# Kernel optimization log

Measured on AMD Instinct MI355X. Metric: run time of the kernel, lower is better.

## Reference

```python
import jax, jax.numpy as jnp
import numpy as np

HEADS = 8
DIM_HEAD = 64
SCALE = DIM_HEAD ** -0.5


def setup_inputs() -> dict:
    key = jax.random.key(0)
    ks = jax.random.split(key, 6)
    b, dim, h, w = 8, 512, 64, 64
    ctx_dim, n = 768, 256
    inner = HEADS * DIM_HEAD  # 512
    x = jax.random.normal(ks[0], (b, dim, h, w), jnp.float32)
    context = jax.random.normal(ks[1], (b, n, ctx_dim), jnp.float32)
    # 1x1 convs / linear reduced to [out, in] matrices
    Wq = jax.random.normal(ks[2], (inner, dim), jnp.float32) * 0.02
    Wkv = jax.random.normal(ks[3], (2 * inner, ctx_dim), jnp.float32) * 0.02
    Wout = jax.random.normal(ks[4], (dim, inner), jnp.float32) * 0.02
    bout = jnp.zeros((dim,), jnp.float32)
    return {"x": x, "context": context, "Wq": Wq, "Wkv": Wkv, "Wout": Wout, "bout": bout}


def reference(x, context, Wq, Wkv, Wout, bout):
    b, c, h, w = x.shape
    # to_q: 1x1 conv (no bias) == per-pixel channel matmul
    q = jnp.einsum('bcxy,ec->bexy', x, Wq)              # [b, inner, h, w]
    # rearrange 'b (h d) x y -> b h (x y) d'
    q = q.reshape(b, HEADS, DIM_HEAD, h * w).transpose(0, 1, 3, 2)
    # to_kv: Linear(context_dim -> 2*inner, no bias)
    kv = jnp.einsum('bnc,ec->bne', context, Wkv)        # [b, n, 2*inner]
    k, v = jnp.split(kv, 2, axis=-1)
    # rearrange 'b n (h d) -> b h n d'
    n = context.shape[1]
    k = k.reshape(b, n, HEADS, DIM_HEAD).transpose(0, 2, 1, 3)
    v = v.reshape(b, n, HEADS, DIM_HEAD).transpose(0, 2, 1, 3)
    sim = jnp.einsum('bhid,bhjd->bhij', q, k) * SCALE   # [b, h, hw, n]
    attn = jax.nn.softmax(sim, axis=-1)
    out = jnp.einsum('bhij,bhjd->bhid', attn, v)        # [b, h, hw, d]
    # rearrange 'b h (x y) d -> b (h d) x y'
    out = out.transpose(0, 1, 3, 2).reshape(b, HEADS * DIM_HEAD, h, w)
    # to_out: 1x1 conv with bias, plus residual
    out = jnp.einsum('bexy,ce->bcxy', out, Wout) + bout[None, :, None, None]
    return out + x
```

## Files before the change

### kernel.cpp

```cpp
#include <hip/hip_runtime.h>

typedef unsigned short u16;
typedef __bf16 bf16x8 __attribute__((ext_vector_type(8)));
typedef __bf16 bf16x4 __attribute__((ext_vector_type(4)));
typedef float f32x4 __attribute__((ext_vector_type(4)));

__device__ __forceinline__ u16 f2bf(float f) {
  __bf16 h = (__bf16)f;
  return *(u16*)&h;
}

__device__ __forceinline__ f32x4 mfma16(bf16x8 a, bf16x8 b, f32x4 c) {
  return __builtin_amdgcn_mfma_f32_16x16x32_bf16(a, b, c, 0, 0, 0);
}

__device__ __forceinline__ void async16(void* lds, const void* g) {
  __builtin_amdgcn_global_load_lds(
      (const __attribute__((address_space(1))) unsigned int*)g,
      (__attribute__((address_space(3))) unsigned int*)lds, 16, 0, 0);
}

#define QSCALE 0.18033688011112042f

__global__ __launch_bounds__(256) void prep_cast(
    const float* __restrict__ Wq, const float* __restrict__ Wkv,
    const float* __restrict__ Wout, const float* __restrict__ ctx,
    u16* __restrict__ Wq_b, u16* __restrict__ Wkv_b,
    u16* __restrict__ Wout_b, u16* __restrict__ ctx_b) {
  const long NWQ = 512L * 512, NWKV = 1024L * 768, NWOUT = 512L * 512, NCTX = 2048L * 768;
  const long total = NWQ + NWKV + NWOUT + NCTX;
  long stride = (long)gridDim.x * 256;
  for (long i = (long)blockIdx.x * 256 + threadIdx.x; i < total; i += stride) {
    long j = i;
    if (j < NWQ) { Wq_b[j] = f2bf(Wq[j] * QSCALE); continue; }
    j -= NWQ;
    if (j < NWKV) { Wkv_b[j] = f2bf(Wkv[j]); continue; }
    j -= NWKV;
    if (j < NWOUT) { Wout_b[j] = f2bf(Wout[j]); continue; }
    j -= NWOUT;
    ctx_b[j] = f2bf(ctx[j]);
  }
}

__global__ __launch_bounds__(256) void transpose_x(const float* __restrict__ x,
                                                   u16* __restrict__ xT) {
  __shared__ float tile[64][65];
  const int b = blockIdx.z, p0 = blockIdx.x * 64, c0 = blockIdx.y * 64;
  const int tx = threadIdx.x & 63, ty = threadIdx.x >> 6;
  const float* xb = x + (long)b * (512L * 4096);
  #pragma unroll
  for (int i = ty; i < 64; i += 4)
    tile[i][tx] = xb[(long)(c0 + i) * 4096 + p0 + tx];
  __syncthreads();
  u16* xTb = xT + (long)b * (4096L * 512);
  #pragma unroll
  for (int i = ty; i < 64; i += 4)
    xTb[(long)(p0 + i) * 512 + c0 + tx] = f2bf(tile[tx][i]);
}

__global__ __launch_bounds__(256) void transpose_v(const u16* __restrict__ kv,
                                                   u16* __restrict__ vT) {
  __shared__ u16 tile[64][65];
  const int b = blockIdx.z, e0 = blockIdx.x * 64, n0 = blockIdx.y * 64;
  const int tx = threadIdx.x & 63, ty = threadIdx.x >> 6;
  #pragma unroll
  for (int i = ty; i < 64; i += 4)
    tile[i][tx] = kv[(long)(b * 256 + n0 + i) * 1024 + 512 + e0 + tx];
  __syncthreads();
  #pragma unroll
  for (int i = ty; i < 64; i += 4)
    vT[(long)b * (512L * 256) + (long)(e0 + i) * 256 + n0 + tx] = tile[tx][i];
}

__global__ __launch_bounds__(256) void gemm_nt128(
    const u16* __restrict__ A, const u16* __restrict__ B, u16* __restrict__ C,
    int M, int N, int K) {
  __shared__ u16 ldsA[2][128 * 64];
  __shared__ u16 ldsB[2][128 * 64];
  const int t = threadIdx.x, wv = t >> 6, ln = t & 63;
  const int m0 = blockIdx.x * 128, n0 = blockIdx.y * 128;
  const int wr = wv >> 1, wc = wv & 1, fr = ln & 15, fq = ln >> 4;

  const u16* aSrc[4];
  const u16* bSrc[4];
  int lbase[4];
  #pragma unroll
  for (int i = 0; i < 4; i++) {
    int c = i * 256 + wv * 64 + ln;
    int row = c >> 3, slot = (c & 7) ^ (row & 7);
    aSrc[i] = A + (long)(m0 + row) * K + slot * 8;
    bSrc[i] = B + (long)(n0 + row) * K + slot * 8;
    lbase[i] = (i * 256 + wv * 64) * 8;
  }

  f32x4 acc[4][4] = {};
  const int nk = K >> 6;
  int cur = 0;

  #pragma unroll
  for (int i = 0; i < 4; i++) {
    async16(&ldsA[0][lbase[i]], aSrc[i]);
    async16(&ldsB[0][lbase[i]], bSrc[i]);
  }

  for (int kt = 0; kt < nk; ++kt) {
    __syncthreads();
    if (kt + 1 < nk) {
      const int ko = (kt + 1) * 64;
      #pragma unroll
      for (int i = 0; i < 4; i++) {
        async16(&ldsA[cur ^ 1][lbase[i]], aSrc[i] + ko);
        async16(&ldsB[cur ^ 1][lbase[i]], bSrc[i] + ko);
      }
    }
    const char* Ab = (const char*)ldsA[cur];
    const char* Bb = (const char*)ldsB[cur];
    #pragma unroll
    for (int kk = 0; kk < 2; ++kk) {
      bf16x8 a[4], b[4];
      #pragma unroll
      for (int mf = 0; mf < 4; ++mf) {
        int row = wr * 64 + mf * 16 + fr;
        a[mf] = *(const bf16x8*)(Ab + row * 128 +
                                 ((kk * 64 + fq * 16) ^ ((row & 7) << 4)));
      }
      #pragma unroll
      for (int nf = 0; nf < 4; ++nf) {
        int row = wc * 64 + nf * 16 + fr;
        b[nf] = *(const bf16x8*)(Bb + row * 128 +
                                 ((kk * 64 + fq * 16) ^ ((row & 7) << 4)));
      }
      #pragma unroll
      for (int mf = 0; mf < 4; ++mf)
        #pragma unroll
        for (int nf = 0; nf < 4; ++nf)
          acc[mf][nf] = mfma16(a[mf], b[nf], acc[mf][nf]);
    }
    cur ^= 1;
  }

  #pragma unroll
  for (int mf = 0; mf < 4; ++mf)
    #pragma unroll
    for (int r = 0; r < 4; ++r) {
      int grow = m0 + wr * 64 + mf * 16 + fq * 4 + r;
      #pragma unroll
      for (int nf = 0; nf < 4; ++nf) {
        int gcol = n0 + wc * 64 + nf * 16 + fr;
        C[(long)grow * N + gcol] = f2bf(acc[mf][nf][r]);
      }
    }
}

template <int EPI>
__global__ __launch_bounds__(512, 2) void gemm_nt256(
    const u16* __restrict__ A, const u16* __restrict__ B, void* __restrict__ Cv,
    int M, int N, int K, long aStrideZ, long bStrideZ, long cStrideZ,
    const float* __restrict__ bias, const float* __restrict__ resid) {
  __shared__ u16 ldsA[2][256 * 64];
  __shared__ u16 ldsB[2][256 * 64];
  const int t = threadIdx.x, wv = t >> 6, ln = t & 63;
  const int m0 = blockIdx.x * 256, n0 = blockIdx.y * 256, z = blockIdx.z;
  const u16* Az = A + (long)z * aStrideZ;
  const u16* Bz = B + (long)z * bStrideZ;
  const int wr = wv >> 2, wc = wv & 3, fr = ln & 15, fq = ln >> 4;

  const u16* aSrc[4];
  const u16* bSrc[4];
  int lbase[4];
  #pragma unroll
  for (int i = 0; i < 4; i++) {
    int c = i * 512 + wv * 64 + ln;
    int row = c >> 3, slot = (c & 7) ^ (row & 7);
    aSrc[i] = Az + (long)(m0 + row) * K + slot * 8;
    bSrc[i] = Bz + (long)(n0 + row) * K + slot * 8;
    lbase[i] = (i * 512 + wv * 64) * 8;
  }

  f32x4 acc[8][4] = {};
  const int nk = K >> 6;
  int cur = 0;

  #pragma unroll
  for (int i = 0; i < 4; i++) {
    async16(&ldsA[0][lbase[i]], aSrc[i]);
    async16(&ldsB[0][lbase[i]], bSrc[i]);
  }

  for (int kt = 0; kt < nk; ++kt) {
    if (kt + 1 < nk) {
      const int ko = (kt + 1) * 64;
      #pragma unroll
      for (int i = 0; i < 4; i++) {
        async16(&ldsA[cur ^ 1][lbase[i]], aSrc[i] + ko);
        async16(&ldsB[cur ^ 1][lbase[i]], bSrc[i] + ko);
      }
      asm volatile("s_waitcnt vmcnt(8)" ::: "memory");
    } else {
      asm volatile("s_waitcnt vmcnt(0)" ::: "memory");
    }
    __builtin_amdgcn_s_barrier();
    __builtin_amdgcn_sched_barrier(0);

    const char* Ab = (const char*)ldsA[cur];
    const char* Bb = (const char*)ldsB[cur];
    #pragma unroll
    for (int kk = 0; kk < 2; ++kk) {
      bf16x8 a[8], b[4];
      #pragma unroll
      for (int mf = 0; mf < 8; ++mf) {
        int row = wr * 128 + mf * 16 + fr;
        a[mf] = *(const bf16x8*)(Ab + row * 128 +
                                 ((kk * 64 + fq * 16) ^ ((row & 7) << 4)));
      }
      #pragma unroll
      for (int nf = 0; nf < 4; ++nf) {
        int row = wc * 64 + nf * 16 + fr;
        b[nf] = *(const bf16x8*)(Bb + row * 128 +
                                 ((kk * 64 + fq * 16) ^ ((row & 7) << 4)));
      }
      __builtin_amdgcn_s_setprio(1);
      #pragma unroll
      for (int mf = 0; mf < 8; ++mf)
        #pragma unroll
        for (int nf = 0; nf < 4; ++nf)
          acc[mf][nf] = mfma16(a[mf], b[nf], acc[mf][nf]);
      __builtin_amdgcn_s_setprio(0);
    }

    __builtin_amdgcn_sched_barrier(0);
    __builtin_amdgcn_s_barrier();
    cur ^= 1;
  }

  if (EPI == 0) {
    u16* Cb = (u16*)Cv + (long)z * cStrideZ;
    #pragma unroll
    for (int mf = 0; mf < 8; ++mf)
      #pragma unroll
      for (int r = 0; r < 4; ++r) {
        int grow = m0 + wr * 128 + mf * 16 + fq * 4 + r;
        #pragma unroll
        for (int nf = 0; nf < 4; ++nf) {
          int gcol = n0 + wc * 64 + nf * 16 + fr;
          Cb[(long)grow * N + gcol] = f2bf(acc[mf][nf][r]);
        }
      }
  } else {
    float* Cf = (float*)Cv + (long)z * cStrideZ;
    const float* Rz = resid + (long)z * cStrideZ;
    #pragma unroll
    for (int mf = 0; mf < 8; ++mf)
      #pragma unroll
      for (int r = 0; r < 4; ++r) {
        int grow = m0 + wr * 128 + mf * 16 + fq * 4 + r;
        float bv = bias[grow];
        #pragma unroll
        for (int nf = 0; nf < 4; ++nf) {
          int gcol = n0 + wc * 64 + nf * 16 + fr;
          long idx = (long)grow * N + gcol;
          Cf[idx] = acc[mf][nf][r] + bv + Rz[idx];
        }
      }
  }
}

__global__ __launch_bounds__(512) void attn_kernel(
    const u16* __restrict__ q, const u16* __restrict__ kv,
    const u16* __restrict__ vT, u16* __restrict__ ao) {
  __shared__ u16 klds[256 * 64];
  __shared__ u16 vlds[64 * 256];
  __shared__ u16 plds[128 * 256];
  const int t = threadIdx.x, w = t >> 6, ln = t & 63;
  const int fr = ln & 15, fq = ln >> 4;
  const int p0 = blockIdx.x * 1024, h = blockIdx.y, b = blockIdx.z;

  const u16* kb = kv + (long)b * 256 * 1024 + h * 64;
  const u16* vb = vT + (long)b * (512L * 256) + (long)h * 64 * 256;

  #pragma unroll
  for (int i = 0; i < 4; ++i) {
    int cbase = i * 512 + w * 64;
    int chunk = cbase + ln;
    int row = chunk >> 3, slot = chunk & 7;
    async16(&klds[cbase * 8], kb + (long)row * 1024 + ((slot ^ (row & 7)) << 3));
  }
  #pragma unroll
  for (int i = 0; i < 4; ++i) {
    int cbase = i * 512 + w * 64;
    int chunk = cbase + ln;
    int row = chunk >> 5, slot = chunk & 31;
    async16(&vlds[cbase * 8], vb + (long)row * 256 + ((slot ^ (row & 7)) << 3));
  }
  __syncthreads();

  const char* kraw = (const char*)klds;
  const char* vraw = (const char*)vlds;
  char* praw = (char*)plds;
  const int prowL = w * 16 + fr;
  const int swz = (fr & 7) << 4;

  const u16* qbase = q + ((long)b * 4096 + p0 + w * 16 + fr) * 512 + h * 64;
  bf16x8 qf0 = *(const bf16x8*)&qbase[fq * 8];
  bf16x8 qf1 = *(const bf16x8*)&qbase[32 + fq * 8];

  for (int it = 0; it < 8; ++it) {
    f32x4 s[16] = {};
    __builtin_amdgcn_s_setprio(1);
    #pragma unroll
    for (int nb = 0; nb < 16; ++nb) {
      int n = nb * 16 + fr;
      bf16x8 kf0 = *(const bf16x8*)(kraw + n * 128 + ((fq * 16) ^ swz));
      bf16x8 kf1 = *(const bf16x8*)(kraw + n * 128 + ((64 + fq * 16) ^ swz));
      s[nb] = mfma16(kf0, qf0, s[nb]);
      s[nb] = mfma16(kf1, qf1, s[nb]);
    }
    __builtin_amdgcn_s_setprio(0);

    const u16* qn = qbase + (long)(((it + 1) & 7) * 128) * 512;
    bf16x8 qn0 = *(const bf16x8*)&qn[fq * 8];
    bf16x8 qn1 = *(const bf16x8*)&qn[32 + fq * 8];

    f32x4 mx = s[0];
    #pragma unroll
    for (int nb = 1; nb < 16; ++nb) {
      mx[0] = fmaxf(mx[0], s[nb][0]); mx[1] = fmaxf(mx[1], s[nb][1]);
      mx[2] = fmaxf(mx[2], s[nb][2]); mx[3] = fmaxf(mx[3], s[nb][3]);
    }
    float m = fmaxf(fmaxf(mx[0], mx[1]), fmaxf(mx[2], mx[3]));
    m = fmaxf(m, __shfl_xor(m, 16));
    m = fmaxf(m, __shfl_xor(m, 32));
    f32x4 sm = {0.f, 0.f, 0.f, 0.f};
    #pragma unroll
    for (int nb = 0; nb < 16; ++nb) {
      #pragma unroll
      for (int r = 0; r < 4; ++r)
        s[nb][r] = __builtin_amdgcn_exp2f(s[nb][r] - m);
      sm += s[nb];
    }
    float sum = (sm[0] + sm[1]) + (sm[2] + sm[3]);
    sum += __shfl_xor(sum, 16);
    sum += __shfl_xor(sum, 32);
    float inv = 1.0f / sum;

    #pragma unroll
    for (int nb = 0; nb < 16; ++nb) {
      bf16x4 pk;
      #pragma unroll
      for (int r = 0; r < 4; ++r) pk[r] = (__bf16)s[nb][r];
      *(bf16x4*)(praw + prowL * 512 + ((nb * 32 + fq * 8) ^ swz)) = pk;
    }
    asm volatile("s_waitcnt lgkmcnt(0)" ::: "memory");
    __builtin_amdgcn_sched_barrier(0);

    f32x4 o[4] = {};
    __builtin_amdgcn_s_setprio(1);
    #pragma unroll
    for (int kk2 = 0; kk2 < 8; ++kk2) {
      bf16x8 pf = *(const bf16x8*)(praw + prowL * 512 + ((kk2 * 64 + fq * 16) ^ swz));
      #pragma unroll
      for (int nfd = 0; nfd < 4; ++nfd) {
        bf16x8 vf = *(const bf16x8*)(vraw + (nfd * 16 + fr) * 512 +
                                     ((kk2 * 64 + fq * 16) ^ swz));
        o[nfd] = mfma16(vf, pf, o[nfd]);
      }
    }
    __builtin_amdgcn_s_setprio(0);

    u16* aob = ao + ((long)b * 4096 + p0 + it * 128 + w * 16 + fr) * 512 + h * 64;
    #pragma unroll
    for (int nfd = 0; nfd < 4; ++nfd) {
      bf16x4 ov;
      #pragma unroll
      for (int r = 0; r < 4; ++r) ov[r] = (__bf16)(o[nfd][r] * inv);
      *(bf16x4*)(aob + nfd * 16 + fq * 4) = ov;
    }
    qf0 = qn0;
    qf1 = qn1;
  }
}

extern "C" void kernel_launch(void* const* d_in, const int* in_sizes, int n_in,
                              void* d_out, int out_size, void* d_ws, size_t ws_size,
                              hipStream_t stream) {
  const float* x    = (const float*)d_in[0];
  const float* ctx  = (const float*)d_in[1];
  const float* Wq   = (const float*)d_in[2];
  const float* Wkv  = (const float*)d_in[3];
  const float* Wout = (const float*)d_in[4];
  const float* bout = (const float*)d_in[5];
  float* out = (float*)d_out;
  char* ws = (char*)d_ws;

  u16* xT     = (u16*)(ws);
  u16* q      = (u16*)(ws + 33554432);
  u16* kv     = (u16*)(ws + 67108864);
  u16* vT     = (u16*)(ws + 71303168);
  u16* Wq_b   = (u16*)(ws + 73400320);
  u16* Wkv_b  = (u16*)(ws + 73924608);
  u16* Wout_b = (u16*)(ws + 75497472);
  u16* ctx_b  = (u16*)(ws + 76021760);
  u16* ao     = xT;

  prep_cast<<<dim3(1024), dim3(256), 0, stream>>>(Wq, Wkv, Wout, ctx,
                                                  Wq_b, Wkv_b, Wout_b, ctx_b);
  transpose_x<<<dim3(64, 8, 8), dim3(256), 0, stream>>>(x, xT);
  gemm_nt256<0><<<dim3(16, 2, 8), dim3(512), 0, stream>>>(
      xT, Wq_b, (void*)q, 4096, 512, 512, 4096L * 512, 0L, 4096L * 512,
      nullptr, nullptr);
  gemm_nt128<<<dim3(16, 8, 1), dim3(256), 0, stream>>>(
      ctx_b, Wkv_b, kv, 2048, 1024, 768);
  transpose_v<<<dim3(8, 4, 8), dim3(256), 0, stream>>>(kv, vT);
  attn_kernel<<<dim3(4, 8, 8), dim3(512), 0, stream>>>(q, kv, vT, ao);
  gemm_nt256<1><<<dim3(2, 16, 8), dim3(512), 0, stream>>>(
      Wout_b, ao, (void*)out, 512, 4096, 512, 0L, 4096L * 512, 512L * 4096,
      bout, x);
}
```

Measured before the change: 141.1 us.

## Interleave async prefetch with MFMA sub-steps and remap GEMM blocks to 1D grid

Restructures the 256x256 GEMM main loop so that the next tile's global-to-LDS loads are issued in four chunks, interleaved with four sub-steps of MFMA work over 32-row slices of A, with barriers between sub-steps. B fragments are loaded once per k-tile and reused. It also replaces the 3D grid with a 1D grid where the batch index is the fastest-varying and paired tiles are adjacent, aiming for better cache/XCD locality. The extra barriers per k-tile add synchronisation cost, and waiting with vmcnt(2) only works if the load ordering assumptions hold.

```diff
diff --git a/kernel.cpp b/kernel.cpp
--- a/kernel.cpp
+++ b/kernel.cpp
@@ -152,7 +152,7 @@
     }
 }
 
-template <int EPI>
+template <int EPI, int PAIRX>
 __global__ __launch_bounds__(512, 2) void gemm_nt256(
     const u16* __restrict__ A, const u16* __restrict__ B, void* __restrict__ Cv,
     int M, int N, int K, long aStrideZ, long bStrideZ, long cStrideZ,
@@ -160,7 +160,14 @@
   __shared__ u16 ldsA[2][256 * 64];
   __shared__ u16 ldsB[2][256 * 64];
   const int t = threadIdx.x, wv = t >> 6, ln = t & 63;
-  const int m0 = blockIdx.x * 256, n0 = blockIdx.y * 256, z = blockIdx.z;
+
+  const int L = blockIdx.x;
+  const int z = L & 7;
+  const int kq = L >> 3;
+  const int pr = kq & 1, ld = kq >> 1;
+  const int m0 = (PAIRX ? pr : ld) * 256;
+  const int n0 = (PAIRX ? ld : pr) * 256;
+
   const u16* Az = A + (long)z * aStrideZ;
   const u16* Bz = B + (long)z * bStrideZ;
   const int wr = wv >> 2, wc = wv & 3, fr = ln & 15, fq = ln >> 4;
@@ -188,48 +195,56 @@
   }
 
   for (int kt = 0; kt < nk; ++kt) {
-    if (kt + 1 < nk) {
-      const int ko = (kt + 1) * 64;
-      #pragma unroll
-      for (int i = 0; i < 4; i++) {
-        async16(&ldsA[cur ^ 1][lbase[i]], aSrc[i] + ko);
-        async16(&ldsB[cur ^ 1][lbase[i]], bSrc[i] + ko);
-      }
-      asm volatile("s_waitcnt vmcnt(8)" ::: "memory");
-    } else {
-      asm volatile("s_waitcnt vmcnt(0)" ::: "memory");
-    }
-    __builtin_amdgcn_s_barrier();
-    __builtin_amdgcn_sched_barrier(0);
-
     const char* Ab = (const char*)ldsA[cur];
     const char* Bb = (const char*)ldsB[cur];
-    #pragma unroll
-    for (int kk = 0; kk < 2; ++kk) {
-      bf16x8 a[8], b[4];
-      #pragma unroll
-      for (int mf = 0; mf < 8; ++mf) {
-        int row = wr * 128 + mf * 16 + fr;
-        a[mf] = *(const bf16x8*)(Ab + row * 128 +
-                                 ((kk * 64 + fq * 16) ^ ((row & 7) << 4)));
-      }
-      #pragma unroll
-      for (int nf = 0; nf < 4; ++nf) {
-        int row = wc * 64 + nf * 16 + fr;
-        b[nf] = *(const bf16x8*)(Bb + row * 128 +
-                                 ((kk * 64 + fq * 16) ^ ((row & 7) << 4)));
-      }
+    const bool pf = (kt + 1 < nk);
+    const int ko = (kt + 1) * 64;
+    bf16x8 b[2][4];
+
+    #pragma unroll
+    for (int d = 0; d < 4; ++d) {
+      if (pf) {
+        async16(&ldsA[cur ^ 1][lbase[d]], aSrc[d] + ko);
+        async16(&ldsB[cur ^ 1][lbase[d]], bSrc[d] + ko);
+      }
+      if (d == 0) {
+        if (pf) asm volatile("s_waitcnt vmcnt(2)" ::: "memory");
+        else    asm volatile("s_waitcnt vmcnt(0)" ::: "memory");
+        __builtin_amdgcn_s_barrier();
+        __builtin_amdgcn_sched_barrier(0);
+        #pragma unroll
+        for (int kk = 0; kk < 2; ++kk)
+          #pragma unroll
+          for (int nf = 0; nf < 4; ++nf) {
+            int row = wc * 64 + nf * 16 + fr;
+            b[kk][nf] = *(const bf16x8*)(Bb + row * 128 +
+                                         ((kk * 64 + fq * 16) ^ ((row & 7) << 4)));
+          }
+      }
+      bf16x8 a[2][2];
+      #pragma unroll
+      for (int kk = 0; kk < 2; ++kk)
+        #pragma unroll
+        for (int qd = 0; qd < 2; ++qd) {
+          int row = wr * 128 + d * 32 + qd * 16 + fr;
+          a[kk][qd] = *(const bf16x8*)(Ab + row * 128 +
+                                       ((kk * 64 + fq * 16) ^ ((row & 7) << 4)));
+        }
+      if (d != 0) __builtin_amdgcn_s_barrier();
+      asm volatile("s_waitcnt lgkmcnt(0)" ::: "memory");
+      __builtin_amdgcn_sched_barrier(0);
       __builtin_amdgcn_s_setprio(1);
       #pragma unroll
-      for (int mf = 0; mf < 8; ++mf)
-        #pragma unroll
-        for (int nf = 0; nf < 4; ++nf)
-          acc[mf][nf] = mfma16(a[mf], b[nf], acc[mf][nf]);
+      for (int kk = 0; kk < 2; ++kk)
+        #pragma unroll
+        for (int qd = 0; qd < 2; ++qd)
+          #pragma unroll
+          for (int nf = 0; nf < 4; ++nf)
+            acc[d * 2 + qd][nf] = mfma16(a[kk][qd], b[kk][nf], acc[d * 2 + qd][nf]);
       __builtin_amdgcn_s_setprio(0);
-    }
-
-    __builtin_amdgcn_sched_barrier(0);
-    __builtin_amdgcn_s_barrier();
+      __builtin_amdgcn_sched_barrier(0);
+      __builtin_amdgcn_s_barrier();
+    }
     cur ^= 1;
   }
 
@@ -405,14 +420,14 @@
   prep_cast<<<dim3(1024), dim3(256), 0, stream>>>(Wq, Wkv, Wout, ctx,
                                                   Wq_b, Wkv_b, Wout_b, ctx_b);
   transpose_x<<<dim3(64, 8, 8), dim3(256), 0, stream>>>(x, xT);
-  gemm_nt256<0><<<dim3(16, 2, 8), dim3(512), 0, stream>>>(
+  gemm_nt256<0, 0><<<dim3(256), dim3(512), 0, stream>>>(
       xT, Wq_b, (void*)q, 4096, 512, 512, 4096L * 512, 0L, 4096L * 512,
       nullptr, nullptr);
   gemm_nt128<<<dim3(16, 8, 1), dim3(256), 0, stream>>>(
       ctx_b, Wkv_b, kv, 2048, 1024, 768);
   transpose_v<<<dim3(8, 4, 8), dim3(256), 0, stream>>>(kv, vT);
   attn_kernel<<<dim3(4, 8, 8), dim3(512), 0, stream>>>(q, kv, vT, ao);
-  gemm_nt256<1><<<dim3(2, 16, 8), dim3(512), 0, stream>>>(
+  gemm_nt256<1, 1><<<dim3(256), dim3(512), 0, stream>>>(
       Wout_b, ao, (void*)out, 512, 4096, 512, 0L, 4096L * 512, 512L * 4096,
       bout, x);
 }
```

Measured after the change: 153.3 us. 8.6% more time.

## Replace 256x256 GEMM with weight-stationary register-resident 128x128 tile kernel

Applied to the files above, without the earlier changes.

Both 1x1-conv GEMMs (Q projection and output projection) now use a new kernel. Each wave keeps its 16-row slice of the weight matrix in registers, so only the activation tile is streamed through double-buffered LDS. Tiles shrink to 128x128 with 1024 blocks and up to 4 blocks per CU, which raises occupancy and parallelism and halves the LDS footprint. In exchange each block does less compute per barrier, weights are re-read from global/L2 by every block, and the output-projection epilogue writes with a different access pattern.

```diff
diff --git a/kernel.cpp b/kernel.cpp
--- a/kernel.cpp
+++ b/kernel.cpp
@@ -153,84 +153,87 @@
 }
 
 template <int EPI>
-__global__ __launch_bounds__(512, 2) void gemm_nt256(
-    const u16* __restrict__ A, const u16* __restrict__ B, void* __restrict__ Cv,
-    int M, int N, int K, long aStrideZ, long bStrideZ, long cStrideZ,
+__global__ __launch_bounds__(512, 4) void gemm_ws(
+    const u16* __restrict__ S, const u16* __restrict__ W, void* __restrict__ Cv,
+    long sStrideZ, long cStrideZ,
     const float* __restrict__ bias, const float* __restrict__ resid) {
-  __shared__ u16 ldsA[2][256 * 64];
-  __shared__ u16 ldsB[2][256 * 64];
+  __shared__ u16 slds[2][128 * 64];
   const int t = threadIdx.x, wv = t >> 6, ln = t & 63;
-  const int m0 = blockIdx.x * 256, n0 = blockIdx.y * 256, z = blockIdx.z;
-  const u16* Az = A + (long)z * aStrideZ;
-  const u16* Bz = B + (long)z * bStrideZ;
-  const int wr = wv >> 2, wc = wv & 3, fr = ln & 15, fq = ln >> 4;
-
-  const u16* aSrc[4];
-  const u16* bSrc[4];
-  int lbase[4];
-  #pragma unroll
-  for (int i = 0; i < 4; i++) {
+  const int fr = ln & 15, fq = ln >> 4;
+
+  const int L = blockIdx.x;
+  const int z = L & 7;
+  const int r_ = L >> 3;
+  const int eg = r_ & 3, pt = r_ >> 2;
+  const int p0 = pt * 128, e0 = eg * 128;
+  const int ew0 = e0 + wv * 16;
+
+  const u16* Sz = S + (long)z * sStrideZ;
+  const u16* wrow = W + (long)(ew0 + fr) * 512;
+
+  const u16* sSrc[2];
+  int lbase[2];
+  #pragma unroll
+  for (int i = 0; i < 2; i++) {
     int c = i * 512 + wv * 64 + ln;
     int row = c >> 3, slot = (c & 7) ^ (row & 7);
-    aSrc[i] = Az + (long)(m0 + row) * K + slot * 8;
-    bSrc[i] = Bz + (long)(n0 + row) * K + slot * 8;
+    sSrc[i] = Sz + (long)(p0 + row) * 512 + slot * 8;
     lbase[i] = (i * 512 + wv * 64) * 8;
   }
 
-  f32x4 acc[8][4] = {};
-  const int nk = K >> 6;
+  f32x4 acc[8] = {};
   int cur = 0;
 
   #pragma unroll
-  for (int i = 0; i < 4; i++) {
-    async16(&ldsA[0][lbase[i]], aSrc[i]);
-    async16(&ldsB[0][lbase[i]], bSrc[i]);
-  }
-
-  for (int kt = 0; kt < nk; ++kt) {
-    if (kt + 1 < nk) {
-      const int ko = (kt + 1) * 64;
-      #pragma unroll
-      for (int i = 0; i < 4; i++) {
-        async16(&ldsA[cur ^ 1][lbase[i]], aSrc[i] + ko);
-        async16(&ldsB[cur ^ 1][lbase[i]], bSrc[i] + ko);
-      }
-      asm volatile("s_waitcnt vmcnt(8)" ::: "memory");
-    } else {
-      asm volatile("s_waitcnt vmcnt(0)" ::: "memory");
-    }
-    __builtin_amdgcn_s_barrier();
-    __builtin_amdgcn_sched_barrier(0);
-
-    const char* Ab = (const char*)ldsA[cur];
-    const char* Bb = (const char*)ldsB[cur];
-    #pragma unroll
-    for (int kk = 0; kk < 2; ++kk) {
-      bf16x8 a[8], b[4];
-      #pragma unroll
-      for (int mf = 0; mf < 8; ++mf) {
-        int row = wr * 128 + mf * 16 + fr;
-        a[mf] = *(const bf16x8*)(Ab + row * 128 +
-                                 ((kk * 64 + fq * 16) ^ ((row & 7) << 4)));
-      }
-      #pragma unroll
-      for (int nf = 0; nf < 4; ++nf) {
-        int row = wc * 64 + nf * 16 + fr;
-        b[nf] = *(const bf16x8*)(Bb + row * 128 +
-                                 ((kk * 64 + fq * 16) ^ ((row & 7) << 4)));
-      }
-      __builtin_amdgcn_s_setprio(1);
-      #pragma unroll
-      for (int mf = 0; mf < 8; ++mf)
+  for (int i = 0; i < 2; i++) async16(&slds[0][lbase[i]], sSrc[i]);
+
+  #pragma unroll
+  for (int half = 0; half < 2; ++half) {
+    bf16x8 wf[4][2];
+    #pragma unroll
+    for (int kc2 = 0; kc2 < 4; ++kc2)
+      #pragma unroll
+      for (int kk = 0; kk < 2; ++kk)
+        wf[kc2][kk] = *(const bf16x8*)&wrow[(half * 4 + kc2) * 64 + kk * 32 + fq * 8];
+
+    #pragma unroll
+    for (int kc2 = 0; kc2 < 4; ++kc2) {
+      const int gkc = half * 4 + kc2;
+      if (gkc < 7) {
+        const int ko = (gkc + 1) * 64;
         #pragma unroll
-        for (int nf = 0; nf < 4; ++nf)
-          acc[mf][nf] = mfma16(a[mf], b[nf], acc[mf][nf]);
-      __builtin_amdgcn_s_setprio(0);
-    }
-
-    __builtin_amdgcn_sched_barrier(0);
-    __builtin_amdgcn_s_barrier();
-    cur ^= 1;
+        for (int i = 0; i < 2; i++)
+          async16(&slds[cur ^ 1][lbase[i]], sSrc[i] + ko);
+        if (kc2 == 0) asm volatile("s_waitcnt vmcnt(10)" ::: "memory");
+        else          asm volatile("s_waitcnt vmcnt(2)" ::: "memory");
+      } else {
+        asm volatile("s_waitcnt vmcnt(0)" ::: "memory");
+      }
+      __builtin_amdgcn_s_barrier();
+      __builtin_amdgcn_sched_barrier(0);
+
+      const char* Sb = (const char*)slds[cur];
+      #pragma unroll
+      for (int kk = 0; kk < 2; ++kk) {
+        bf16x8 sf[8];
+        #pragma unroll
+        for (int mf = 0; mf < 8; ++mf) {
+          int row = mf * 16 + fr;
+          sf[mf] = *(const bf16x8*)(Sb + row * 128 +
+                                    ((kk * 64 + fq * 16) ^ ((row & 7) << 4)));
+        }
+        __builtin_amdgcn_s_setprio(1);
+        #pragma unroll
+        for (int mf = 0; mf < 8; ++mf)
+          acc[mf] = (EPI == 0) ? mfma16(sf[mf], wf[kc2][kk], acc[mf])
+                               : mfma16(wf[kc2][kk], sf[mf], acc[mf]);
+        __builtin_amdgcn_s_setprio(0);
+      }
+
+      __builtin_amdgcn_sched_barrier(0);
+      __builtin_amdgcn_s_barrier();
+      cur ^= 1;
+    }
   }
 
   if (EPI == 0) {
@@ -239,29 +242,22 @@
     for (int mf = 0; mf < 8; ++mf)
       #pragma unroll
       for (int r = 0; r < 4; ++r) {
-        int grow = m0 + wr * 128 + mf * 16 + fq * 4 + r;
-        #pragma unroll
-        for (int nf = 0; nf < 4; ++nf) {
-          int gcol = n0 + wc * 64 + nf * 16 + fr;
-          Cb[(long)grow * N + gcol] = f2bf(acc[mf][nf][r]);
-        }
+        int p = p0 + mf * 16 + fq * 4 + r;
+        Cb[(long)p * 512 + ew0 + fr] = f2bf(acc[mf][r]);
       }
   } else {
     float* Cf = (float*)Cv + (long)z * cStrideZ;
     const float* Rz = resid + (long)z * cStrideZ;
-    #pragma unroll
-    for (int mf = 0; mf < 8; ++mf)
-      #pragma unroll
-      for (int r = 0; r < 4; ++r) {
-        int grow = m0 + wr * 128 + mf * 16 + fq * 4 + r;
-        float bv = bias[grow];
-        #pragma unroll
-        for (int nf = 0; nf < 4; ++nf) {
-          int gcol = n0 + wc * 64 + nf * 16 + fr;
-          long idx = (long)grow * N + gcol;
-          Cf[idx] = acc[mf][nf][r] + bv + Rz[idx];
-        }
-      }
+    const int c = ew0 + fq * 4;
+    #pragma unroll
+    for (int r = 0; r < 4; ++r) {
+      float bv = bias[c + r];
+      #pragma unroll
+      for (int mf = 0; mf < 8; ++mf) {
+        long idx = (long)(c + r) * 4096 + p0 + mf * 16 + fr;
+        Cf[idx] = acc[mf][r] + bv + Rz[idx];
+      }
+    }
   }
 }
 
@@ -405,14 +401,12 @@
   prep_cast<<<dim3(1024), dim3(256), 0, stream>>>(Wq, Wkv, Wout, ctx,
                                                   Wq_b, Wkv_b, Wout_b, ctx_b);
   transpose_x<<<dim3(64, 8, 8), dim3(256), 0, stream>>>(x, xT);
-  gemm_nt256<0><<<dim3(16, 2, 8), dim3(512), 0, stream>>>(
-      xT, Wq_b, (void*)q, 4096, 512, 512, 4096L * 512, 0L, 4096L * 512,
-      nullptr, nullptr);
+  gemm_ws<0><<<dim3(1024), dim3(512), 0, stream>>>(
+      xT, Wq_b, (void*)q, 4096L * 512, 4096L * 512, nullptr, nullptr);
   gemm_nt128<<<dim3(16, 8, 1), dim3(256), 0, stream>>>(
       ctx_b, Wkv_b, kv, 2048, 1024, 768);
   transpose_v<<<dim3(8, 4, 8), dim3(256), 0, stream>>>(kv, vT);
   attn_kernel<<<dim3(4, 8, 8), dim3(512), 0, stream>>>(q, kv, vT, ao);
-  gemm_nt256<1><<<dim3(2, 16, 8), dim3(512), 0, stream>>>(
-      Wout_b, ao, (void*)out, 512, 4096, 512, 0L, 4096L * 512, 512L * 4096,
-      bout, x);
-}
+  gemm_ws<1><<<dim3(1024), dim3(512), 0, stream>>>(
+      ao, Wout_b, (void*)out, 4096L * 512, 512L * 4096, bout, x);
+}
```

Measured after the change: 151.4 us. 1.07x slower.

## Merge prep kernels and fuse Q and KV projections into one GEMM launch

Applied to the files above, without the earlier changes.

Merges the weight/context cast and the x transpose into a single launch that splits work by block index. Folds the Q projection and the KV projection into one 256x256-tile GEMM launch of 288 blocks, and moves the KV GEMM from 128-tiles to 256-tiles. Block order in the Q and output GEMMs is remapped so the batch index varies fastest, which may change L2 locality. This cuts kernel launches and lets the small KV GEMM overlap with the Q GEMM, at the cost of uneven per-block work (K=768 vs 512) in one grid.

```diff
diff --git a/kernel.cpp b/kernel.cpp
--- a/kernel.cpp
+++ b/kernel.cpp
@@ -22,30 +22,33 @@
 
 #define QSCALE 0.18033688011112042f
 
-__global__ __launch_bounds__(256) void prep_cast(
-    const float* __restrict__ Wq, const float* __restrict__ Wkv,
-    const float* __restrict__ Wout, const float* __restrict__ ctx,
+__global__ __launch_bounds__(256) void prep_transpose(
+    const float* __restrict__ x, const float* __restrict__ Wq,
+    const float* __restrict__ Wkv, const float* __restrict__ Wout,
+    const float* __restrict__ ctx, u16* __restrict__ xT,
     u16* __restrict__ Wq_b, u16* __restrict__ Wkv_b,
     u16* __restrict__ Wout_b, u16* __restrict__ ctx_b) {
-  const long NWQ = 512L * 512, NWKV = 1024L * 768, NWOUT = 512L * 512, NCTX = 2048L * 768;
-  const long total = NWQ + NWKV + NWOUT + NCTX;
-  long stride = (long)gridDim.x * 256;
-  for (long i = (long)blockIdx.x * 256 + threadIdx.x; i < total; i += stride) {
-    long j = i;
-    if (j < NWQ) { Wq_b[j] = f2bf(Wq[j] * QSCALE); continue; }
-    j -= NWQ;
-    if (j < NWKV) { Wkv_b[j] = f2bf(Wkv[j]); continue; }
-    j -= NWKV;
-    if (j < NWOUT) { Wout_b[j] = f2bf(Wout[j]); continue; }
-    j -= NWOUT;
-    ctx_b[j] = f2bf(ctx[j]);
-  }
-}
-
-__global__ __launch_bounds__(256) void transpose_x(const float* __restrict__ x,
-                                                   u16* __restrict__ xT) {
   __shared__ float tile[64][65];
-  const int b = blockIdx.z, p0 = blockIdx.x * 64, c0 = blockIdx.y * 64;
+  int bx = blockIdx.x;
+  if (bx < 1024) {
+    const long NWQ = 512L * 512, NWKV = 1024L * 768, NWOUT = 512L * 512,
+               NCTX = 2048L * 768;
+    const long total = NWQ + NWKV + NWOUT + NCTX;
+    long stride = 1024L * 256;
+    for (long i = (long)bx * 256 + threadIdx.x; i < total; i += stride) {
+      long j = i;
+      if (j < NWQ) { Wq_b[j] = f2bf(Wq[j] * QSCALE); continue; }
+      j -= NWQ;
+      if (j < NWKV) { Wkv_b[j] = f2bf(Wkv[j]); continue; }
+      j -= NWKV;
+      if (j < NWOUT) { Wout_b[j] = f2bf(Wout[j]); continue; }
+      j -= NWOUT;
+      ctx_b[j] = f2bf(ctx[j]);
+    }
+    return;
+  }
+  bx -= 1024;
+  const int p0 = (bx & 63) * 64, c0 = ((bx >> 6) & 7) * 64, b = bx >> 9;
   const int tx = threadIdx.x & 63, ty = threadIdx.x >> 6;
   const float* xb = x + (long)b * (512L * 4096);
   #pragma unroll
@@ -72,113 +75,50 @@
     vT[(long)b * (512L * 256) + (long)(e0 + i) * 256 + n0 + tx] = tile[tx][i];
 }
 
-__global__ __launch_bounds__(256) void gemm_nt128(
-    const u16* __restrict__ A, const u16* __restrict__ B, u16* __restrict__ C,
-    int M, int N, int K) {
-  __shared__ u16 ldsA[2][128 * 64];
-  __shared__ u16 ldsB[2][128 * 64];
+__global__ __launch_bounds__(512, 2) void gemm_qkv(
+    const u16* __restrict__ xT, const u16* __restrict__ Wq,
+    u16* __restrict__ q, const u16* __restrict__ ctxb,
+    const u16* __restrict__ Wkv, u16* __restrict__ kvout) {
+  __shared__ u16 ldsA[2][256 * 64];
+  __shared__ u16 ldsB[2][256 * 64];
   const int t = threadIdx.x, wv = t >> 6, ln = t & 63;
-  const int m0 = blockIdx.x * 128, n0 = blockIdx.y * 128;
-  const int wr = wv >> 1, wc = wv & 1, fr = ln & 15, fq = ln >> 4;
+  const int wr = wv >> 2, wc = wv & 3, fr = ln & 15, fq = ln >> 4;
+
+  const int L = blockIdx.x;
+  const u16 *A, *B;
+  u16* C;
+  int N, K, nk, m0, n0;
+  if (L < 256) {
+    const int z = L & 7, kq = L >> 3, pr = kq & 1, ld = kq >> 1;
+    m0 = ld * 256;
+    n0 = pr * 256;
+    A = xT + (long)z * (4096L * 512);
+    B = Wq;
+    C = q + (long)z * (4096L * 512);
+    N = 512; K = 512; nk = 8;
+  } else {
+    const int l2 = L - 256;
+    m0 = (l2 & 7) * 256;
+    n0 = (l2 >> 3) * 256;
+    A = ctxb;
+    B = Wkv;
+    C = kvout;
+    N = 1024; K = 768; nk = 12;
+  }
 
   const u16* aSrc[4];
   const u16* bSrc[4];
   int lbase[4];
   #pragma unroll
   for (int i = 0; i < 4; i++) {
-    int c = i * 256 + wv * 64 + ln;
+    int c = i * 512 + wv * 64 + ln;
     int row = c >> 3, slot = (c & 7) ^ (row & 7);
     aSrc[i] = A + (long)(m0 + row) * K + slot * 8;
     bSrc[i] = B + (long)(n0 + row) * K + slot * 8;
-    lbase[i] = (i * 256 + wv * 64) * 8;
-  }
-
-  f32x4 acc[4][4] = {};
-  const int nk = K >> 6;
-  int cur = 0;
-
-  #pragma unroll
-  for (int i = 0; i < 4; i++) {
-    async16(&ldsA[0][lbase[i]], aSrc[i]);
-    async16(&ldsB[0][lbase[i]], bSrc[i]);
-  }
-
-  for (int kt = 0; kt < nk; ++kt) {
-    __syncthreads();
-    if (kt + 1 < nk) {
-      const int ko = (kt + 1) * 64;
-      #pragma unroll
-      for (int i = 0; i < 4; i++) {
-        async16(&ldsA[cur ^ 1][lbase[i]], aSrc[i] + ko);
-        async16(&ldsB[cur ^ 1][lbase[i]], bSrc[i] + ko);
-      }
-    }
-    const char* Ab = (const char*)ldsA[cur];
-    const char* Bb = (const char*)ldsB[cur];
-    #pragma unroll
-    for (int kk = 0; kk < 2; ++kk) {
-      bf16x8 a[4], b[4];
-      #pragma unroll
-      for (int mf = 0; mf < 4; ++mf) {
-        int row = wr * 64 + mf * 16 + fr;
-        a[mf] = *(const bf16x8*)(Ab + row * 128 +
-                                 ((kk * 64 + fq * 16) ^ ((row & 7) << 4)));
-      }
-      #pragma unroll
-      for (int nf = 0; nf < 4; ++nf) {
-        int row = wc * 64 + nf * 16 + fr;
-        b[nf] = *(const bf16x8*)(Bb + row * 128 +
-                                 ((kk * 64 + fq * 16) ^ ((row & 7) << 4)));
-      }
-      #pragma unroll
-      for (int mf = 0; mf < 4; ++mf)
-        #pragma unroll
-        for (int nf = 0; nf < 4; ++nf)
-          acc[mf][nf] = mfma16(a[mf], b[nf], acc[mf][nf]);
-    }
-    cur ^= 1;
-  }
-
-  #pragma unroll
-  for (int mf = 0; mf < 4; ++mf)
-    #pragma unroll
-    for (int r = 0; r < 4; ++r) {
-      int grow = m0 + wr * 64 + mf * 16 + fq * 4 + r;
-      #pragma unroll
-      for (int nf = 0; nf < 4; ++nf) {
-        int gcol = n0 + wc * 64 + nf * 16 + fr;
-        C[(long)grow * N + gcol] = f2bf(acc[mf][nf][r]);
-      }
-    }
-}
-
-template <int EPI>
-__global__ __launch_bounds__(512, 2) void gemm_nt256(
-    const u16* __restrict__ A, const u16* __restrict__ B, void* __restrict__ Cv,
-    int M, int N, int K, long aStrideZ, long bStrideZ, long cStrideZ,
-    const float* __restrict__ bias, const float* __restrict__ resid) {
-  __shared__ u16 ldsA[2][256 * 64];
-  __shared__ u16 ldsB[2][256 * 64];
-  const int t = threadIdx.x, wv = t >> 6, ln = t & 63;
-  const int m0 = blockIdx.x * 256, n0 = blockIdx.y * 256, z = blockIdx.z;
-  const u16* Az = A + (long)z * aStrideZ;
-  const u16* Bz = B + (long)z * bStrideZ;
-  const int wr = wv >> 2, wc = wv & 3, fr = ln & 15, fq = ln >> 4;
-
-  const u16* aSrc[4];
-  const u16* bSrc[4];
-  int lbase[4];
-  #pragma unroll
-  for (int i = 0; i < 4; i++) {
-    int c = i * 512 + wv * 64 + ln;
-    int row = c >> 3, slot = (c & 7) ^ (row & 7);
-    aSrc[i] = Az + (long)(m0 + row) * K + slot * 8;
-    bSrc[i] = Bz + (long)(n0 + row) * K + slot * 8;
     lbase[i] = (i * 512 + wv * 64) * 8;
   }
 
   f32x4 acc[8][4] = {};
-  const int nk = K >> 6;
   int cur = 0;
 
   #pragma unroll
@@ -233,36 +173,119 @@
     cur ^= 1;
   }
 
-  if (EPI == 0) {
-    u16* Cb = (u16*)Cv + (long)z * cStrideZ;
-    #pragma unroll
-    for (int mf = 0; mf < 8; ++mf)
-      #pragma unroll
-      for (int r = 0; r < 4; ++r) {
-        int grow = m0 + wr * 128 + mf * 16 + fq * 4 + r;
+  #pragma unroll
+  for (int mf = 0; mf < 8; ++mf)
+    #pragma unroll
+    for (int r = 0; r < 4; ++r) {
+      int grow = m0 + wr * 128 + mf * 16 + fq * 4 + r;
+      #pragma unroll
+      for (int nf = 0; nf < 4; ++nf) {
+        int gcol = n0 + wc * 64 + nf * 16 + fr;
+        C[(long)grow * N + gcol] = f2bf(acc[mf][nf][r]);
+      }
+    }
+}
+
+__global__ __launch_bounds__(512, 2) void gemm_out(
+    const u16* __restrict__ Wout, const u16* __restrict__ ao,
+    float* __restrict__ out, const float* __restrict__ bias,
+    const float* __restrict__ resid) {
+  __shared__ u16 ldsA[2][256 * 64];
+  __shared__ u16 ldsB[2][256 * 64];
+  const int t = threadIdx.x, wv = t >> 6, ln = t & 63;
+  const int wr = wv >> 2, wc = wv & 3, fr = ln & 15, fq = ln >> 4;
+
+  const int L = blockIdx.x;
+  const int z = L & 7, kq = L >> 3, pr = kq & 1, ld = kq >> 1;
+  const int m0 = pr * 256;
+  const int n0 = ld * 256;
+  const int N = 4096, K = 512, nk = 8;
+
+  const u16* A = Wout;
+  const u16* B = ao + (long)z * (4096L * 512);
+
+  const u16* aSrc[4];
+  const u16* bSrc[4];
+  int lbase[4];
+  #pragma unroll
+  for (int i = 0; i < 4; i++) {
+    int c = i * 512 + wv * 64 + ln;
+    int row = c >> 3, slot = (c & 7) ^ (row & 7);
+    aSrc[i] = A + (long)(m0 + row) * K + slot * 8;
+    bSrc[i] = B + (long)(n0 + row) * K + slot * 8;
+    lbase[i] = (i * 512 + wv * 64) * 8;
+  }
+
+  f32x4 acc[8][4] = {};
+  int cur = 0;
+
+  #pragma unroll
+  for (int i = 0; i < 4; i++) {
+    async16(&ldsA[0][lbase[i]], aSrc[i]);
+    async16(&ldsB[0][lbase[i]], bSrc[i]);
+  }
+
+  for (int kt = 0; kt < nk; ++kt) {
+    if (kt + 1 < nk) {
+      const int ko = (kt + 1) * 64;
+      #pragma unroll
+      for (int i = 0; i < 4; i++) {
+        async16(&ldsA[cur ^ 1][lbase[i]], aSrc[i] + ko);
+        async16(&ldsB[cur ^ 1][lbase[i]], bSrc[i] + ko);
+      }
+      asm volatile("s_waitcnt vmcnt(8)" ::: "memory");
+    } else {
+      asm volatile("s_waitcnt vmcnt(0)" ::: "memory");
+    }
+    __builtin_amdgcn_s_barrier();
+    __builtin_amdgcn_sched_barrier(0);
+
+    const char* Ab = (const char*)ldsA[cur];
+    const char* Bb = (const char*)ldsB[cur];
+    #pragma unroll
+    for (int kk = 0; kk < 2; ++kk) {
+      bf16x8 a[8], b[4];
+      #pragma unroll
+      for (int mf = 0; mf < 8; ++mf) {
+        int row = wr * 128 + mf * 16 + fr;
+        a[mf] = *(const bf16x8*)(Ab + row * 128 +
+                                 ((kk * 64 + fq * 16) ^ ((row & 7) << 4)));
+      }
+      #pragma unroll
+      for (int nf = 0; nf < 4; ++nf) {
+        int row = wc * 64 + nf * 16 + fr;
+        b[nf] = *(const bf16x8*)(Bb + row * 128 +
+                                 ((kk * 64 + fq * 16) ^ ((row & 7) << 4)));
+      }
+      __builtin_amdgcn_s_setprio(1);
+      #pragma unroll
+      for (int mf = 0; mf < 8; ++mf)
         #pragma unroll
-        for (int nf = 0; nf < 4; ++nf) {
-          int gcol = n0 + wc * 64 + nf * 16 + fr;
-          Cb[(long)grow * N + gcol] = f2bf(acc[mf][nf][r]);
-        }
-      }
-  } else {
-    float* Cf = (float*)Cv + (long)z * cStrideZ;
-    const float* Rz = resid + (long)z * cStrideZ;
-    #pragma unroll
-    for (int mf = 0; mf < 8; ++mf)
-      #pragma unroll
-      for (int r = 0; r < 4; ++r) {
-        int grow = m0 + wr * 128 + mf * 16 + fq * 4 + r;
-        float bv = bias[grow];
-        #pragma unroll
-        for (int nf = 0; nf < 4; ++nf) {
-          int gcol = n0 + wc * 64 + nf * 16 + fr;
-          long idx = (long)grow * N + gcol;
-          Cf[idx] = acc[mf][nf][r] + bv + Rz[idx];
-        }
-      }
-  }
+        for (int nf = 0; nf < 4; ++nf)
+          acc[mf][nf] = mfma16(a[mf], b[nf], acc[mf][nf]);
+      __builtin_amdgcn_s_setprio(0);
+    }
+
+    __builtin_amdgcn_sched_barrier(0);
+    __builtin_amdgcn_s_barrier();
+    cur ^= 1;
+  }
+
+  float* Cf = out + (long)z * (512L * 4096);
+  const float* Rz = resid + (long)z * (512L * 4096);
+  #pragma unroll
+  for (int mf = 0; mf < 8; ++mf)
+    #pragma unroll
+    for (int r = 0; r < 4; ++r) {
+      int grow = m0 + wr * 128 + mf * 16 + fq * 4 + r;
+      float bv = bias[grow];
+      #pragma unroll
+      for (int nf = 0; nf < 4; ++nf) {
+        int gcol = n0 + wc * 64 + nf * 16 + fr;
+        long idx = (long)grow * N + gcol;
+        Cf[idx] = acc[mf][nf][r] + bv + Rz[idx];
+      }
+    }
 }
 
 __global__ __launch_bounds__(512) void attn_kernel(
@@ -402,17 +425,12 @@
   u16* ctx_b  = (u16*)(ws + 76021760);
   u16* ao     = xT;
 
-  prep_cast<<<dim3(1024), dim3(256), 0, stream>>>(Wq, Wkv, Wout, ctx,
-                                                  Wq_b, Wkv_b, Wout_b, ctx_b);
-  transpose_x<<<dim3(64, 8, 8), dim3(256), 0, stream>>>(x, xT);
-  gemm_nt256<0><<<dim3(16, 2, 8), dim3(512), 0, stream>>>(
-      xT, Wq_b, (void*)q, 4096, 512, 512, 4096L * 512, 0L, 4096L * 512,
-      nullptr, nullptr);
-  gemm_nt128<<<dim3(16, 8, 1), dim3(256), 0, stream>>>(
-      ctx_b, Wkv_b, kv, 2048, 1024, 768);
+  prep_transpose<<<dim3(5120), dim3(256), 0, stream>>>(
+      x, Wq, Wkv, Wout, ctx, xT, Wq_b, Wkv_b, Wout_b, ctx_b);
+  gemm_qkv<<<dim3(288), dim3(512), 0, stream>>>(
+      xT, Wq_b, q, ctx_b, Wkv_b, kv);
   transpose_v<<<dim3(8, 4, 8), dim3(256), 0, stream>>>(kv, vT);
   attn_kernel<<<dim3(4, 8, 8), dim3(512), 0, stream>>>(q, kv, vT, ao);
-  gemm_nt256<1><<<dim3(2, 16, 8), dim3(512), 0, stream>>>(
-      Wout_b, ao, (void*)out, 512, 4096, 512, 0L, 4096L * 512, 512L * 4096,
-      bout, x);
-}
+  gemm_out<<<dim3(256), dim3(512), 0, stream>>>(
+      Wout_b, ao, out, bout, x);
+}
```

After: 137.9 us. 2.3% less time.
